# Kernel tuning notes

Hardware: AMD Instinct MI355X
Metric: run time of the kernel (lower is better)

The kernel has to match this reference:

```python
import jax, jax.numpy as jnp
import numpy as np

B, SQ, SK, D, DV = 16, 2048, 2048, 128, 128
NUM_HEADS = 2
DROPOUT_P = 0.1
SCALE_FACTOR = 1.0 / (DROPOUT_P * NUM_HEADS)  # = 5.0; scores are divided by this


def setup_inputs() -> dict:
    key = jax.random.key(0)
    k1, k2, k3, k4 = jax.random.split(key, 4)
    x1 = jax.random.normal(k1, (B, SQ, D), dtype=jnp.float32)
    x2 = jax.random.normal(k2, (B, SK, D), dtype=jnp.float32)
    x3 = jax.random.normal(k3, (B, SK, DV), dtype=jnp.float32)
    # deterministic dropout keep-mask (True -> keep), keep prob = 1 - p
    drop_mask = jax.random.bernoulli(k4, 1.0 - DROPOUT_P, (B, SQ, SK))
    return {"x1": x1, "x2": x2, "x3": x3, "drop_mask": drop_mask}


def reference(x1, x2, x3, drop_mask):
    # v1 = x1 @ x2^T : [B, Sq, Sk]
    scores = jnp.einsum("bqd,bkd->bqk", x1, x2)
    # v2 = v1 / scale_factor (scale_factor = 1/(p*heads) = 5 -> multiply by 0.2)
    scores = scores * (1.0 / SCALE_FACTOR)
    probs = jax.nn.softmax(scores, axis=-1)
    # dropout with inverted scaling 1/(1-p)
    keep_scale = 1.0 / (1.0 - DROPOUT_P)
    probs = jnp.where(drop_mask, probs * keep_scale, 0.0)
    # output = probs @ x3 : [B, Sq, Dv]
    return jnp.einsum("bqk,bkv->bqv", probs, x3)
```

## Files before the change

kernel.cpp:

```cpp
#include <hip/hip_runtime.h>
#include <stdint.h>


#define B_   16
#define SQ_  2048
#define SK_  2048
#define D_   128
#define DV_  128
#define BK   64
#define NT   (SK_ / BK)

typedef short  s16x8 __attribute__((ext_vector_type(8)));
typedef float  f32x4 __attribute__((ext_vector_type(4)));
typedef unsigned int u32x4 __attribute__((ext_vector_type(4)));
typedef unsigned short u16;
typedef unsigned int   u32;
typedef unsigned char  u8;

__device__ __forceinline__ u32 pk2(float a, float b) {
    u32 r;
    asm("v_cvt_pk_bf16_f32 %0, %1, %2" : "=v"(r) : "v"(a), "v"(b));
    return r;
}
__device__ __forceinline__ u16 f2bf(float f) { return (u16)pk2(f, 0.0f); }

__device__ __forceinline__ void gload16(void* lds, const void* g) {
    __builtin_amdgcn_global_load_lds((const __attribute__((address_space(1))) u32*)g,
                                     (__attribute__((address_space(3))) u32*)lds,
                                     16, 0, 0);
}

__global__ __launch_bounds__(256)
void prep_k(const float* __restrict__ Kg, u16* __restrict__ Kz)
{
    int g   = blockIdx.x * 256 + threadIdx.x;
    int b   = g >> 15;
    int rem = g & 32767;
    int k   = rem >> 4;
    int grp = rem & 15;
    const float* src = Kg + ((size_t)b * SK_ + k) * D_ + grp * 8;
    float4 x = *(const float4*)(src);
    float4 y = *(const float4*)(src + 4);
    u32x4 w = { pk2(x.x, x.y), pk2(x.z, x.w), pk2(y.x, y.y), pk2(y.z, y.w) };
    int c = (grp * 8) ^ ((k & 7) << 3);
    *(u32x4*)(&Kz[((size_t)b * SK_ + k) * D_ + c]) = w;
}

__global__ __launch_bounds__(256)
void prep_v(const float* __restrict__ Vg, u16* __restrict__ Vz)
{
    int g  = blockIdx.x * 256 + threadIdx.x;
    int dv = g & 127;
    int kg = (g >> 7) & 7;
    int kt = (g >> 10) & 31;
    int b  = g >> 15;
    const float* src = Vg + ((size_t)b * SK_ + kt * 64 + kg * 8) * DV_ + dv;
    float v[8];
    #pragma unroll
    for (int jj = 0; jj < 8; ++jj) v[jj] = src[(size_t)jj * DV_];
    u32x4 w = { pk2(v[0], v[1]), pk2(v[2], v[3]), pk2(v[4], v[5]), pk2(v[6], v[7]) };
    int c = (kg * 8) ^ ((dv & 7) << 3);
    *(u32x4*)(&Vz[(((size_t)b * 32 + kt) * 128 + dv) * 64 + c]) = w;
}

__global__ __launch_bounds__(256)
void prep_m(const int* __restrict__ Mg, u8* __restrict__ Mp)
{
    const int bid  = blockIdx.x;
    const int b    = bid >> 6;
    const int qt   = bid & 63;
    const int tid  = threadIdx.x;
    const int wave = tid >> 6;
    const int lane = tid & 63;
    const int n16  = lane & 15;
    const int quad = lane >> 4;
    const int qh   = wave & 1;
    const int kh   = wave >> 1;

    const int* base = Mg + ((size_t)(b * SQ_ + qt * 32 + qh * 16 + quad * 4)) * SK_
                    + kh * 32 + n16;
    u8* out = Mp + (size_t)bid * 8192 + tid;

    #pragma unroll 4
    for (int kt = 0; kt < 32; ++kt) {
        u32 m = 0;
        #pragma unroll
        for (int t = 0; t < 2; ++t)
            #pragma unroll
            for (int r = 0; r < 4; ++r)
                m |= (base[(size_t)r * SK_ + kt * 64 + t * 16] != 0 ? 1u : 0u) << (t * 4 + r);
        out[(size_t)kt * 256] = (u8)m;
    }
}

#define STEP(IT, CUR, NXT)                                                    \
  {                                                                           \
    if ((IT) + 1 < NT) {        \
      const u16* Kt = Kz + kvbase + (size_t)((IT) + 1) * 8192;                \
      const u16* Vt = Vz + kvbase + (size_t)((IT) + 1) * 8192;                \
      _Pragma("unroll")                                                       \
      for (int i = 0; i < 4; ++i) {                                           \
        int c16 = (wave * 4 + i) * 512;                                       \
        gload16(&Kbuf[NXT][c16], &Kt[c16 + lane * 8]);                        \
        gload16(&Vbuf[NXT][c16], &Vt[c16 + lane * 8]);                        \
      }                                                                       \
    }                                                                         \
    u32 mb = (u32)Ms[(IT) * 256 + tid];          \
    f32x4 s[2];                                                               \
    s[0] = (f32x4){0.f, 0.f, 0.f, 0.f};                                       \
    s[1] = (f32x4){0.f, 0.f, 0.f, 0.f};                                       \
    __builtin_amdgcn_s_setprio(1);                                            \
    _Pragma("unroll")                                                         \
    for (int kb = 0; kb < 4; ++kb) {                                          \
      _Pragma("unroll")                                                       \
      for (int t = 0; t < 2; ++t) {                                           \
        int kcol = kh * 32 + t * 16 + n16;                                    \
        int coff = (kb * 32 + quad * 8) ^ ((kcol & 7) << 3);                  \
        s16x8 bK = *(const s16x8*)(&Kbuf[CUR][kcol * 128 + coff]);            \
        s[t] = __builtin_amdgcn_mfma_f32_16x16x32_bf16(aQ[kb], bK, s[t], 0, 0, 0); \
      }                                                                       \
    }                                                                         \
    __builtin_amdgcn_s_setprio(0);                                            \
    _Pragma("unroll")                                                         \
    for (int t = 0; t < 2; ++t)                                               \
      _Pragma("unroll")                                                       \
      for (int r = 0; r < 4; ++r) {                                           \
        float p = __expf(fmaf(s[t][r], 0.2f, -12.0f));                        \
        l_part[r] += p;                                   \
        float pv = ((mb >> (t * 4 + r)) & 1u) ? p : 0.f;                      \
        Ps[wave * 640 + (quad * 4 + r) * 40 + t * 16 + n16] = f2bf(pv);       \
      }                                                                       \
    s16x8 aP = *(const s16x8*)(&Ps[wave * 640 + n16 * 40 + quad * 8]);        \
    __builtin_amdgcn_s_setprio(1);                                            \
    _Pragma("unroll")                                                         \
    for (int nt = 0; nt < 8; ++nt) {                                          \
      int dv = nt * 16 + n16;                                                 \
      int coff = (kh * 32 + quad * 8) ^ ((dv & 7) << 3);                      \
      s16x8 bV = *(const s16x8*)(&Vbuf[CUR][dv * 64 + coff]);                 \
      o[nt] = __builtin_amdgcn_mfma_f32_16x16x32_bf16(aP, bV, o[nt], 0, 0, 0); \
    }                                                                         \
    __builtin_amdgcn_s_setprio(0);                                            \
    __syncthreads();    \
  }

__global__ __launch_bounds__(256, 2)
void fattn_main(const float* __restrict__ Qg, const u16* __restrict__ Kz,
                const u16* __restrict__ Vz, const u8* __restrict__ Mp,
                float* __restrict__ Og)
{
    __shared__ __align__(16) u16 Kbuf[2][64 * 128];
    __shared__ __align__(16) u16 Vbuf[2][128 * 64];
    __shared__ __align__(16) u16 Ps[4 * 16 * 40];
    __shared__ __align__(16) u8  Ms[32 * 256];
    __shared__ float lxch[32];

    const int tid  = threadIdx.x;
    const int wave = tid >> 6;
    const int lane = tid & 63;
    const int n16  = lane & 15;
    const int quad = lane >> 4;
    const int qh   = wave & 1;
    const int kh   = wave >> 1;

    const int raw = blockIdx.x;
    const int xcd = raw & 7;
    const int j   = raw >> 3;
    const int b   = xcd * 2 + (j & 1);
    const int qt  = j >> 1;
    const int q0  = qt << 5;

    {
        const u8* Mpb = Mp + ((size_t)(b * 64 + qt)) * 8192;
        #pragma unroll
        for (int i = 0; i < 2; ++i) {
            int off = (wave * 2 + i) * 1024;
            gload16(&Ms[off], &Mpb[off + lane * 16]);
        }
        const u16* Kt = Kz + (size_t)b * 262144;
        const u16* Vt = Vz + (size_t)b * 262144;
        #pragma unroll
        for (int i = 0; i < 4; ++i) {
            int c16 = (wave * 4 + i) * 512;
            gload16(&Kbuf[0][c16], &Kt[c16 + lane * 8]);
            gload16(&Vbuf[0][c16], &Vt[c16 + lane * 8]);
        }
    }
    s16x8 aQ[4];
    {
        const float* qsrc = Qg + ((size_t)b * SQ_ + q0 + qh * 16 + n16) * D_;
        #pragma unroll
        for (int kb = 0; kb < 4; ++kb) {
            float4 x = *(const float4*)(qsrc + kb * 32 + quad * 8);
            float4 y = *(const float4*)(qsrc + kb * 32 + quad * 8 + 4);
            u32x4 w = { pk2(x.x, x.y), pk2(x.z, x.w), pk2(y.x, y.y), pk2(y.z, y.w) };
            aQ[kb] = __builtin_bit_cast(s16x8, w);
        }
    }

    f32x4 o[8];
    #pragma unroll
    for (int i = 0; i < 8; ++i) o[i] = (f32x4){0.f, 0.f, 0.f, 0.f};
    float l_part[4] = {0.f, 0.f, 0.f, 0.f};

    const size_t kvbase = (size_t)b * 262144;

    __syncthreads();

    for (int it = 0; it < NT; it += 2) {
        STEP(it,     0, 1)
        STEP(it + 1, 1, 0)
    }

    float lr[4];
    #pragma unroll
    for (int r = 0; r < 4; ++r) {
        float l = l_part[r];
        #pragma unroll
        for (int off = 1; off < 16; off <<= 1) l += __shfl_xor(l, off);
        lr[r] = l;
    }
    float* oxch = (float*)Kbuf;
    if (kh == 1) {
        #pragma unroll
        for (int r = 0; r < 4; ++r) {
            int row = qh * 16 + quad * 4 + r;
            #pragma unroll
            for (int nt = 0; nt < 8; ++nt)
                oxch[row * 128 + nt * 16 + n16] = o[nt][r];
            if (n16 == 0) lxch[row] = lr[r];
        }
    }
    __syncthreads();
    if (kh == 0) {
        const float ksc = 1.0f / 0.9f;
        #pragma unroll
        for (int r = 0; r < 4; ++r) {
            int row = qh * 16 + quad * 4 + r;
            float inv = ksc / (lr[r] + lxch[row]);
            size_t ob = ((size_t)b * SQ_ + q0 + row) * (size_t)DV_;
            #pragma unroll
            for (int nt = 0; nt < 8; ++nt)
                Og[ob + nt * 16 + n16] = (o[nt][r] + oxch[row * 128 + nt * 16 + n16]) * inv;
        }
    }
}

#define BQ_FB 64
#define LDQ  136
#define LDK  136
#define LDVT 72
#define LDP  72

__global__ __launch_bounds__(256, 2)
void fattn_fb(const float* __restrict__ Qg, const float* __restrict__ Kg,
              const float* __restrict__ Vg, const int* __restrict__ Mg,
              float* __restrict__ Og)
{
    __shared__ u16 Qs[BQ_FB * LDQ];
    __shared__ u16 Ks[BK * LDK];
    __shared__ u16 Vt[DV_ * LDVT];
    __shared__ u16 Ps[4 * 16 * LDP];

    const int tid  = threadIdx.x;
    const int wave = tid >> 6;
    const int lane = tid & 63;
    const int n16  = lane & 15;
    const int quad = lane >> 4;

    const int raw = blockIdx.x;
    const int xcd = raw & 7;
    const int j   = raw >> 3;
    const int b   = xcd * 2 + (j & 1);
    const int q0  = (j >> 1) << 6;

    const int srow = tid >> 4;
    const int scol = (tid & 15) * 8;
    const int vrot = (tid & 7) * 8;

    {
        const float* src = Qg + ((size_t)b * SQ_ + q0) * D_;
        #pragma unroll
        for (int c = 0; c < 4; ++c) {
            int row = c * 16 + srow;
            float4 v0 = *(const float4*)(&src[row * D_ + scol]);
            float4 v1 = *(const float4*)(&src[row * D_ + scol + 4]);
            uint4 pk = { pk2(v0.x, v0.y), pk2(v0.z, v0.w),
                         pk2(v1.x, v1.y), pk2(v1.z, v1.w) };
            *(uint4*)(&Qs[row * LDQ + scol]) = pk;
        }
    }
    __syncthreads();

    s16x8 aQ[4];
    {
        const int qr = wave * 16 + n16;
        #pragma unroll
        for (int kb = 0; kb < 4; ++kb)
            aQ[kb] = *(const s16x8*)(&Qs[qr * LDQ + kb * 32 + quad * 8]);
    }

    f32x4 o[8];
    #pragma unroll
    for (int i = 0; i < 8; ++i) o[i] = (f32x4){0.f, 0.f, 0.f, 0.f};
    float l_part[4] = {0.f, 0.f, 0.f, 0.f};

    const size_t mask_qbase = ((size_t)b * SQ_ + q0 + wave * 16 + quad * 4) * (size_t)SK_;
    const float* baseK = Kg + ((size_t)b * SK_) * D_;
    const float* baseV = Vg + ((size_t)b * SK_) * DV_;

    float4 kf[8], vf[8];
    #pragma unroll
    for (int c = 0; c < 4; ++c) {
        int row = c * 16 + srow;
        kf[2*c]   = *(const float4*)(&baseK[row * D_ + scol]);
        kf[2*c+1] = *(const float4*)(&baseK[row * D_ + scol + 4]);
        vf[2*c]   = *(const float4*)(&baseV[row * DV_ + scol]);
        vf[2*c+1] = *(const float4*)(&baseV[row * DV_ + scol + 4]);
    }
    int mkc[4][4], mkn[4][4];
    #pragma unroll
    for (int t = 0; t < 4; ++t)
        #pragma unroll
        for (int r = 0; r < 4; ++r)
            mkc[t][r] = Mg[mask_qbase + (size_t)r * SK_ + (t * 16 + n16)];

    for (int it = 0; it < NT; ++it) {
        __syncthreads();
        #pragma unroll
        for (int c = 0; c < 4; ++c) {
            int row = c * 16 + srow;
            uint4 pk = { pk2(kf[2*c].x, kf[2*c].y),     pk2(kf[2*c].z, kf[2*c].w),
                         pk2(kf[2*c+1].x, kf[2*c+1].y), pk2(kf[2*c+1].z, kf[2*c+1].w) };
            *(uint4*)(&Ks[row * LDK + scol]) = pk;
        }
        #pragma unroll
        for (int c = 0; c < 4; ++c) {
            int k    = c * 16 + srow;
            int rcol = (k + vrot) & 63;
            int dv0  = scol;
            u32 r0 = pk2(vf[2*c].x,   vf[2*c].y);
            u32 r1 = pk2(vf[2*c].z,   vf[2*c].w);
            u32 r2 = pk2(vf[2*c+1].x, vf[2*c+1].y);
            u32 r3 = pk2(vf[2*c+1].z, vf[2*c+1].w);
            Vt[(dv0 + 0) * LDVT + rcol] = (u16)r0;
            Vt[(dv0 + 1) * LDVT + rcol] = (u16)(r0 >> 16);
            Vt[(dv0 + 2) * LDVT + rcol] = (u16)r1;
            Vt[(dv0 + 3) * LDVT + rcol] = (u16)(r1 >> 16);
            Vt[(dv0 + 4) * LDVT + rcol] = (u16)r2;
            Vt[(dv0 + 5) * LDVT + rcol] = (u16)(r2 >> 16);
            Vt[(dv0 + 6) * LDVT + rcol] = (u16)r3;
            Vt[(dv0 + 7) * LDVT + rcol] = (u16)(r3 >> 16);
        }
        if (it + 1 < NT) {
            const int k0n = (it + 1) * BK;
            #pragma unroll
            for (int c = 0; c < 4; ++c) {
                int row = k0n + c * 16 + srow;
                kf[2*c]   = *(const float4*)(&baseK[row * D_ + scol]);
                kf[2*c+1] = *(const float4*)(&baseK[row * D_ + scol + 4]);
                vf[2*c]   = *(const float4*)(&baseV[row * DV_ + scol]);
                vf[2*c+1] = *(const float4*)(&baseV[row * DV_ + scol + 4]);
            }
            #pragma unroll
            for (int t = 0; t < 4; ++t)
                #pragma unroll
                for (int r = 0; r < 4; ++r)
                    mkn[t][r] = Mg[mask_qbase + (size_t)r * SK_ + (k0n + t * 16 + n16)];
        }
        __syncthreads();

        f32x4 s[4];
        #pragma unroll
        for (int t = 0; t < 4; ++t) s[t] = (f32x4){0.f, 0.f, 0.f, 0.f};
        #pragma unroll
        for (int kb = 0; kb < 4; ++kb) {
            #pragma unroll
            for (int t = 0; t < 4; ++t) {
                s16x8 bK = *(const s16x8*)(&Ks[(t * 16 + n16) * LDK + kb * 32 + quad * 8]);
                s[t] = __builtin_amdgcn_mfma_f32_16x16x32_bf16(aQ[kb], bK, s[t], 0, 0, 0);
            }
        }
        #pragma unroll
        for (int t = 0; t < 4; ++t)
            #pragma unroll
            for (int r = 0; r < 4; ++r) {
                float p = __expf(fmaf(s[t][r], 0.2f, -12.0f));
                l_part[r] += p;
                float pv = mkc[t][r] ? p : 0.f;
                Ps[(wave * 16 + quad * 4 + r) * LDP + t * 16 + n16] = f2bf(pv);
            }
        #pragma unroll
        for (int kk = 0; kk < 2; ++kk) {
            s16x8 aP = *(const s16x8*)(&Ps[(wave * 16 + n16) * LDP + kk * 32 + quad * 8]);
            #pragma unroll
            for (int nt = 0; nt < 8; ++nt) {
                int dv   = nt * 16 + n16;
                int rcol = (kk * 32 + quad * 8 + 8 * ((dv >> 3) & 7)) & 63;
                s16x8 bV = *(const s16x8*)(&Vt[dv * LDVT + rcol]);
                o[nt] = __builtin_amdgcn_mfma_f32_16x16x32_bf16(aP, bV, o[nt], 0, 0, 0);
            }
        }
        #pragma unroll
        for (int t = 0; t < 4; ++t)
            #pragma unroll
            for (int r = 0; r < 4; ++r) mkc[t][r] = mkn[t][r];
    }

    const float keep_scale = 1.0f / 0.9f;
    #pragma unroll
    for (int r = 0; r < 4; ++r) {
        float l = l_part[r];
        #pragma unroll
        for (int off = 1; off < 16; off <<= 1)
            l += __shfl_xor(l, off);
        float inv_l = keep_scale / l;
        size_t obase = ((size_t)b * SQ_ + q0 + wave * 16 + quad * 4 + r) * DV_;
        #pragma unroll
        for (int nt = 0; nt < 8; ++nt)
            Og[obase + nt * 16 + n16] = o[nt][r] * inv_l;
    }
}

extern "C" void kernel_launch(void* const* d_in, const int* in_sizes, int n_in,
                              void* d_out, int out_size, void* d_ws, size_t ws_size,
                              hipStream_t stream) {
    const float* Qg = (const float*)d_in[0];
    const float* Kg = (const float*)d_in[1];
    const float* Vg = (const float*)d_in[2];
    const int*   Mg = (const int*)d_in[3];
    float* Og = (float*)d_out;
    if (d_ws != nullptr && ws_size >= (size_t)24 * 1024 * 1024) {
        u16* Kz = (u16*)d_ws;
        u16* Vz = Kz + 4194304;
        u8*  Mp = (u8*)(Vz + 4194304);
        prep_k<<<dim3(2048), 256, 0, stream>>>(Kg, Kz);
        prep_v<<<dim3(2048), 256, 0, stream>>>(Vg, Vz);
        prep_m<<<dim3(1024), 256, 0, stream>>>(Mg, Mp);
        fattn_main<<<dim3(1024), 256, 0, stream>>>(Qg, Kz, Vz, Mp, Og);
    } else {
        fattn_fb<<<dim3(512), 256, 0, stream>>>(Qg, Kg, Vg, Mg, Og);
    }
}
```

Before: 484.0 us.

## Double query tile per block and read dropout mask directly in attention kernel

Removes the separate mask-packing kernel and its byte-packed workspace. The main kernel now loads the int32 dropout mask straight from global memory into registers, prefetching one KV tile ahead. Each wave now handles two 16-row query subtiles (64 query rows per block, 512 blocks), so every K/V tile loaded into LDS is reused across twice as many queries. The cost is more registers per thread (two sets of accumulators and mask values) and scattered 4-byte mask loads inside the loop, which may reduce occupancy or stall on global memory.

```diff
diff --git a/kernel.cpp b/kernel.cpp
--- a/kernel.cpp
+++ b/kernel.cpp
@@ -15,7 +15,6 @@
 typedef unsigned int u32x4 __attribute__((ext_vector_type(4)));
 typedef unsigned short u16;
 typedef unsigned int   u32;
-typedef unsigned char  u8;
 
 __device__ __forceinline__ u32 pk2(float a, float b) {
     u32 r;
@@ -63,121 +62,126 @@
     *(u32x4*)(&Vz[(((size_t)b * 32 + kt) * 128 + dv) * 64 + c]) = w;
 }
 
-__global__ __launch_bounds__(256)
-void prep_m(const int* __restrict__ Mg, u8* __restrict__ Mp)
+#define STEP(IT, CUR, NXT, MC, MN)                                            \
+  {                                                                           \
+    if ((IT) + 1 < NT) {      \
+      const u16* Kt = Kz + kvbase + (size_t)((IT) + 1) * 8192;                \
+      const u16* Vt = Vz + kvbase + (size_t)((IT) + 1) * 8192;                \
+      _Pragma("unroll")                                                       \
+      for (int i = 0; i < 4; ++i) {                                           \
+        int c16 = (wave * 4 + i) * 512;                                       \
+        gload16(&Kbuf[NXT][c16], &Kt[c16 + lane * 8]);                        \
+        gload16(&Vbuf[NXT][c16], &Vt[c16 + lane * 8]);                        \
+      }                                                                       \
+      _Pragma("unroll")                                                       \
+      for (int qs = 0; qs < 2; ++qs)                                          \
+        _Pragma("unroll")                                                     \
+        for (int t = 0; t < 2; ++t)                                           \
+          _Pragma("unroll")                                                   \
+          for (int r = 0; r < 4; ++r)                                         \
+            MN[qs][t][r] = mbase[(size_t)(qs * 16 + r) * SK_                  \
+                                 + ((IT) + 1) * 64 + t * 16];                 \
+    }                                                                         \
+    f32x4 s[2][2];                                                            \
+    _Pragma("unroll")                                                         \
+    for (int qs = 0; qs < 2; ++qs)                                            \
+      _Pragma("unroll")                                                       \
+      for (int t = 0; t < 2; ++t) s[qs][t] = (f32x4){0.f, 0.f, 0.f, 0.f};     \
+    __builtin_amdgcn_s_setprio(1);                                            \
+    _Pragma("unroll")                                                         \
+    for (int kb = 0; kb < 4; ++kb) {                                          \
+      _Pragma("unroll")                                                       \
+      for (int t = 0; t < 2; ++t) {                                           \
+        int kcol = wk * 32 + t * 16 + n16;                                    \
+        int coff = (kb * 32 + quad * 8) ^ ((kcol & 7) << 3);                  \
+        s16x8 bK = *(const s16x8*)(&Kbuf[CUR][kcol * 128 + coff]);            \
+        _Pragma("unroll")                                                     \
+        for (int qs = 0; qs < 2; ++qs)                                        \
+          s[qs][t] = __builtin_amdgcn_mfma_f32_16x16x32_bf16(aQ[qs][kb], bK,  \
+                                                             s[qs][t], 0, 0, 0); \
+      }                                                                       \
+    }                                                                         \
+    __builtin_amdgcn_s_setprio(0);                                            \
+    _Pragma("unroll")                                                         \
+    for (int qs = 0; qs < 2; ++qs)                                            \
+      _Pragma("unroll")                                                       \
+      for (int t = 0; t < 2; ++t)                                             \
+        _Pragma("unroll")                                                     \
+        for (int r = 0; r < 4; ++r) {                                         \
+          float p = __expf(fmaf(s[qs][t][r], 0.2f, -12.0f));                  \
+          l_part[qs][r] += p;                             \
+          float pv = MC[qs][t][r] ? p : 0.f;                     \
+          Ps[wave * 1280 + (qs * 16 + quad * 4 + r) * 40 + t * 16 + n16] = f2bf(pv); \
+        }                                                                     \
+    __builtin_amdgcn_s_setprio(1);                                            \
+    _Pragma("unroll")                                                         \
+    for (int qs = 0; qs < 2; ++qs) {                                          \
+      s16x8 aP = *(const s16x8*)(&Ps[wave * 1280 + (qs * 16 + n16) * 40 + quad * 8]); \
+      _Pragma("unroll")                                                       \
+      for (int nt = 0; nt < 8; ++nt) {                                        \
+        int dv = nt * 16 + n16;                                               \
+        int coff = (wk * 32 + quad * 8) ^ ((dv & 7) << 3);                    \
+        s16x8 bV = *(const s16x8*)(&Vbuf[CUR][dv * 64 + coff]);               \
+        o[qs][nt] = __builtin_amdgcn_mfma_f32_16x16x32_bf16(aP, bV, o[qs][nt], 0, 0, 0); \
+      }                                                                       \
+    }                                                                         \
+    __builtin_amdgcn_s_setprio(0);                                            \
+    __syncthreads();    \
+  }
+
+__global__ __launch_bounds__(256, 2)
+void fattn_main(const float* __restrict__ Qg, const u16* __restrict__ Kz,
+                const u16* __restrict__ Vz, const int* __restrict__ Mg,
+                float* __restrict__ Og)
 {
-    const int bid  = blockIdx.x;
-    const int b    = bid >> 6;
-    const int qt   = bid & 63;
+    __shared__ __align__(16) u16 Kbuf[2][64 * 128];
+    __shared__ __align__(16) u16 Vbuf[2][128 * 64];
+    __shared__ __align__(16) u16 Ps[4 * 32 * 40];
+    __shared__ float lxch[64];
+
     const int tid  = threadIdx.x;
     const int wave = tid >> 6;
     const int lane = tid & 63;
     const int n16  = lane & 15;
     const int quad = lane >> 4;
-    const int qh   = wave & 1;
-    const int kh   = wave >> 1;
-
-    const int* base = Mg + ((size_t)(b * SQ_ + qt * 32 + qh * 16 + quad * 4)) * SK_
-                    + kh * 32 + n16;
-    u8* out = Mp + (size_t)bid * 8192 + tid;
-
-    #pragma unroll 4
-    for (int kt = 0; kt < 32; ++kt) {
-        u32 m = 0;
-        #pragma unroll
-        for (int t = 0; t < 2; ++t)
-            #pragma unroll
-            for (int r = 0; r < 4; ++r)
-                m |= (base[(size_t)r * SK_ + kt * 64 + t * 16] != 0 ? 1u : 0u) << (t * 4 + r);
-        out[(size_t)kt * 256] = (u8)m;
-    }
-}
-
-#define STEP(IT, CUR, NXT)                                                    \
-  {                                                                           \
-    if ((IT) + 1 < NT) {        \
-      const u16* Kt = Kz + kvbase + (size_t)((IT) + 1) * 8192;                \
-      const u16* Vt = Vz + kvbase + (size_t)((IT) + 1) * 8192;                \
-      _Pragma("unroll")                                                       \
-      for (int i = 0; i < 4; ++i) {                                           \
-        int c16 = (wave * 4 + i) * 512;                                       \
-        gload16(&Kbuf[NXT][c16], &Kt[c16 + lane * 8]);                        \
-        gload16(&Vbuf[NXT][c16], &Vt[c16 + lane * 8]);                        \
-      }                                                                       \
-    }                                                                         \
-    u32 mb = (u32)Ms[(IT) * 256 + tid];          \
-    f32x4 s[2];                                                               \
-    s[0] = (f32x4){0.f, 0.f, 0.f, 0.f};                                       \
-    s[1] = (f32x4){0.f, 0.f, 0.f, 0.f};                                       \
-    __builtin_amdgcn_s_setprio(1);                                            \
-    _Pragma("unroll")                                                         \
-    for (int kb = 0; kb < 4; ++kb) {                                          \
-      _Pragma("unroll")                                                       \
-      for (int t = 0; t < 2; ++t) {                                           \
-        int kcol = kh * 32 + t * 16 + n16;                                    \
-        int coff = (kb * 32 + quad * 8) ^ ((kcol & 7) << 3);                  \
-        s16x8 bK = *(const s16x8*)(&Kbuf[CUR][kcol * 128 + coff]);            \
-        s[t] = __builtin_amdgcn_mfma_f32_16x16x32_bf16(aQ[kb], bK, s[t], 0, 0, 0); \
-      }                                                                       \
-    }                                                                         \
-    __builtin_amdgcn_s_setprio(0);                                            \
-    _Pragma("unroll")                                                         \
-    for (int t = 0; t < 2; ++t)                                               \
-      _Pragma("unroll")                                                       \
-      for (int r = 0; r < 4; ++r) {                                           \
-        float p = __expf(fmaf(s[t][r], 0.2f, -12.0f));                        \
-        l_part[r] += p;                                   \
-        float pv = ((mb >> (t * 4 + r)) & 1u) ? p : 0.f;                      \
-        Ps[wave * 640 + (quad * 4 + r) * 40 + t * 16 + n16] = f2bf(pv);       \
-      }                                                                       \
-    s16x8 aP = *(const s16x8*)(&Ps[wave * 640 + n16 * 40 + quad * 8]);        \
-    __builtin_amdgcn_s_setprio(1);                                            \
-    _Pragma("unroll")                                                         \
-    for (int nt = 0; nt < 8; ++nt) {                                          \
-      int dv = nt * 16 + n16;                                                 \
-      int coff = (kh * 32 + quad * 8) ^ ((dv & 7) << 3);                      \
-      s16x8 bV = *(const s16x8*)(&Vbuf[CUR][dv * 64 + coff]);                 \
-      o[nt] = __builtin_amdgcn_mfma_f32_16x16x32_bf16(aP, bV, o[nt], 0, 0, 0); \
-    }                                                                         \
-    __builtin_amdgcn_s_setprio(0);                                            \
-    __syncthreads();    \
-  }
-
-__global__ __launch_bounds__(256, 2)
-void fattn_main(const float* __restrict__ Qg, const u16* __restrict__ Kz,
-                const u16* __restrict__ Vz, const u8* __restrict__ Mp,
-                float* __restrict__ Og)
-{
-    __shared__ __align__(16) u16 Kbuf[2][64 * 128];
-    __shared__ __align__(16) u16 Vbuf[2][128 * 64];
-    __shared__ __align__(16) u16 Ps[4 * 16 * 40];
-    __shared__ __align__(16) u8  Ms[32 * 256];
-    __shared__ float lxch[32];
-
-    const int tid  = threadIdx.x;
-    const int wave = tid >> 6;
-    const int lane = tid & 63;
-    const int n16  = lane & 15;
-    const int quad = lane >> 4;
-    const int qh   = wave & 1;
-    const int kh   = wave >> 1;
+    const int wq   = wave & 1;
+    const int wk   = wave >> 1;
 
     const int raw = blockIdx.x;
     const int xcd = raw & 7;
     const int j   = raw >> 3;
     const int b   = xcd * 2 + (j & 1);
     const int qt  = j >> 1;
-    const int q0  = qt << 5;
+    const int q0  = qt << 6;
+
+    s16x8 aQ[2][4];
+    #pragma unroll
+    for (int qs = 0; qs < 2; ++qs) {
+        const float* qsrc = Qg + ((size_t)b * SQ_ + q0 + wq * 32 + qs * 16 + n16) * D_;
+        #pragma unroll
+        for (int kb = 0; kb < 4; ++kb) {
+            float4 x = *(const float4*)(qsrc + kb * 32 + quad * 8);
+            float4 y = *(const float4*)(qsrc + kb * 32 + quad * 8 + 4);
+            u32x4 w = { pk2(x.x, x.y), pk2(x.z, x.w), pk2(y.x, y.y), pk2(y.z, y.w) };
+            aQ[qs][kb] = __builtin_bit_cast(s16x8, w);
+        }
+    }
+
+    f32x4 o[2][8];
+    #pragma unroll
+    for (int qs = 0; qs < 2; ++qs)
+        #pragma unroll
+        for (int i = 0; i < 8; ++i) o[qs][i] = (f32x4){0.f, 0.f, 0.f, 0.f};
+    float l_part[2][4] = {{0.f, 0.f, 0.f, 0.f}, {0.f, 0.f, 0.f, 0.f}};
+
+    const size_t kvbase = (size_t)b * 262144;
+
+    const int* mbase = Mg + ((size_t)(b * SQ_ + q0 + wq * 32 + quad * 4)) * SK_
+                     + wk * 32 + n16;
 
     {
-        const u8* Mpb = Mp + ((size_t)(b * 64 + qt)) * 8192;
-        #pragma unroll
-        for (int i = 0; i < 2; ++i) {
-            int off = (wave * 2 + i) * 1024;
-            gload16(&Ms[off], &Mpb[off + lane * 16]);
-        }
-        const u16* Kt = Kz + (size_t)b * 262144;
-        const u16* Vt = Vz + (size_t)b * 262144;
+        const u16* Kt = Kz + kvbase;
+        const u16* Vt = Vz + kvbase;
         #pragma unroll
         for (int i = 0; i < 4; ++i) {
             int c16 = (wave * 4 + i) * 512;
@@ -185,63 +189,60 @@
             gload16(&Vbuf[0][c16], &Vt[c16 + lane * 8]);
         }
     }
-    s16x8 aQ[4];
-    {
-        const float* qsrc = Qg + ((size_t)b * SQ_ + q0 + qh * 16 + n16) * D_;
-        #pragma unroll
-        for (int kb = 0; kb < 4; ++kb) {
-            float4 x = *(const float4*)(qsrc + kb * 32 + quad * 8);
-            float4 y = *(const float4*)(qsrc + kb * 32 + quad * 8 + 4);
-            u32x4 w = { pk2(x.x, x.y), pk2(x.z, x.w), pk2(y.x, y.y), pk2(y.z, y.w) };
-            aQ[kb] = __builtin_bit_cast(s16x8, w);
-        }
-    }
-
-    f32x4 o[8];
-    #pragma unroll
-    for (int i = 0; i < 8; ++i) o[i] = (f32x4){0.f, 0.f, 0.f, 0.f};
-    float l_part[4] = {0.f, 0.f, 0.f, 0.f};
-
-    const size_t kvbase = (size_t)b * 262144;
+    int mA[2][2][4], mB[2][2][4];
+    #pragma unroll
+    for (int qs = 0; qs < 2; ++qs)
+        #pragma unroll
+        for (int t = 0; t < 2; ++t)
+            #pragma unroll
+            for (int r = 0; r < 4; ++r)
+                mA[qs][t][r] = mbase[(size_t)(qs * 16 + r) * SK_ + t * 16];
 
     __syncthreads();
 
     for (int it = 0; it < NT; it += 2) {
-        STEP(it,     0, 1)
-        STEP(it + 1, 1, 0)
-    }
-
-    float lr[4];
-    #pragma unroll
-    for (int r = 0; r < 4; ++r) {
-        float l = l_part[r];
-        #pragma unroll
-        for (int off = 1; off < 16; off <<= 1) l += __shfl_xor(l, off);
-        lr[r] = l;
-    }
+        STEP(it,     0, 1, mA, mB)
+        STEP(it + 1, 1, 0, mB, mA)
+    }
+
+    float lr[2][4];
+    #pragma unroll
+    for (int qs = 0; qs < 2; ++qs)
+        #pragma unroll
+        for (int r = 0; r < 4; ++r) {
+            float l = l_part[qs][r];
+            #pragma unroll
+            for (int off = 1; off < 16; off <<= 1) l += __shfl_xor(l, off);
+            lr[qs][r] = l;
+        }
     float* oxch = (float*)Kbuf;
-    if (kh == 1) {
-        #pragma unroll
-        for (int r = 0; r < 4; ++r) {
-            int row = qh * 16 + quad * 4 + r;
-            #pragma unroll
-            for (int nt = 0; nt < 8; ++nt)
-                oxch[row * 128 + nt * 16 + n16] = o[nt][r];
-            if (n16 == 0) lxch[row] = lr[r];
-        }
+    if (wk == 1) {
+        #pragma unroll
+        for (int qs = 0; qs < 2; ++qs)
+            #pragma unroll
+            for (int r = 0; r < 4; ++r) {
+                int row = wq * 32 + qs * 16 + quad * 4 + r;
+                #pragma unroll
+                for (int nt = 0; nt < 8; ++nt)
+                    oxch[row * 128 + nt * 16 + n16] = o[qs][nt][r];
+                if (n16 == 0) lxch[row] = lr[qs][r];
+            }
     }
     __syncthreads();
-    if (kh == 0) {
+    if (wk == 0) {
         const float ksc = 1.0f / 0.9f;
         #pragma unroll
-        for (int r = 0; r < 4; ++r) {
-            int row = qh * 16 + quad * 4 + r;
-            float inv = ksc / (lr[r] + lxch[row]);
-            size_t ob = ((size_t)b * SQ_ + q0 + row) * (size_t)DV_;
-            #pragma unroll
-            for (int nt = 0; nt < 8; ++nt)
-                Og[ob + nt * 16 + n16] = (o[nt][r] + oxch[row * 128 + nt * 16 + n16]) * inv;
-        }
+        for (int qs = 0; qs < 2; ++qs)
+            #pragma unroll
+            for (int r = 0; r < 4; ++r) {
+                int row = wq * 32 + qs * 16 + quad * 4 + r;
+                float inv = ksc / (lr[qs][r] + lxch[row]);
+                size_t ob = ((size_t)b * SQ_ + q0 + row) * (size_t)DV_;
+                #pragma unroll
+                for (int nt = 0; nt < 8; ++nt)
+                    Og[ob + nt * 16 + n16] =
+                        (o[qs][nt][r] + oxch[row * 128 + nt * 16 + n16]) * inv;
+            }
     }
 }
 
@@ -429,14 +430,12 @@
     const float* Vg = (const float*)d_in[2];
     const int*   Mg = (const int*)d_in[3];
     float* Og = (float*)d_out;
-    if (d_ws != nullptr && ws_size >= (size_t)24 * 1024 * 1024) {
+    if (d_ws != nullptr && ws_size >= (size_t)16 * 1024 * 1024) {
         u16* Kz = (u16*)d_ws;
         u16* Vz = Kz + 4194304;
-        u8*  Mp = (u8*)(Vz + 4194304);
         prep_k<<<dim3(2048), 256, 0, stream>>>(Kg, Kz);
         prep_v<<<dim3(2048), 256, 0, stream>>>(Vg, Vz);
-        prep_m<<<dim3(1024), 256, 0, stream>>>(Mg, Mp);
-        fattn_main<<<dim3(1024), 256, 0, stream>>>(Qg, Kz, Vz, Mp, Og);
+        fattn_main<<<dim3(512), 256, 0, stream>>>(Qg, Kz, Vz, Mg, Og);
     } else {
         fattn_fb<<<dim3(512), 256, 0, stream>>>(Qg, Kg, Vg, Mg, Og);
     }
```

Result: faster. 419.1 us (-13.4%).
